# Kernel tuning notes

Measured on AMD Instinct MI355X. Metric: run time of the kernel, lower is better.

## Reference

```python
import jax, jax.numpy as jnp
import numpy as np

KEEP_RATIO = 0.5
B, H, W = 8, 1024, 1024


def setup_inputs() -> dict:
    key = jax.random.key(0)
    k1, k2, k3 = jax.random.split(key, 3)
    logits = jax.random.normal(k1, (B, 1, H, W), dtype=jnp.float32)
    targets = jax.random.randint(k2, (B, 1, H, W), 0, 2, dtype=jnp.int32)
    tissue_mask = jax.random.randint(k3, (B, 1, H, W), 0, 2, dtype=jnp.int32)
    return {"logits": logits, "targets": targets, "tissue_mask": tissue_mask}


def reference(logits, targets, tissue_mask):
    b = logits.shape[0]
    x = logits.reshape(b, -1)                       # (B, N)
    t = targets.reshape(b, -1).astype(x.dtype)      # {0,1}
    m = tissue_mask.reshape(b, -1).astype(x.dtype)  # {0,1}
    n = x.shape[1]

    # stable binary_cross_entropy_with_logits, reduction='none'
    bce = jnp.maximum(x, 0.0) - x * t + jnp.log1p(jnp.exp(-jnp.abs(x)))
    loss = bce * m                                  # masked per-pixel loss

    pos = t * m                                     # positives inside tissue
    neg = (1.0 - t) * m                             # negatives inside tissue
    n_pos = jnp.sum(pos, axis=1)                    # (B,)
    n_neg = jnp.sum(neg, axis=1)

    k_all = max(1, int(n * KEEP_RATIO))             # static python int
    # kept count per row: all positives + top-(k_all - n_pos) negatives (clamped)
    k_keep = n_pos + jnp.minimum(jnp.maximum(k_all - n_pos, 0.0), n_neg)  # (B,)

    BIG = jnp.asarray(1e30, x.dtype)
    # sort key: positives always first, then negatives by loss, then non-tissue
    sort_key = jnp.where(pos > 0, BIG, jnp.where(neg > 0, loss, -BIG))
    order = jnp.argsort(-sort_key, axis=1)          # descending
    sorted_loss = jnp.take_along_axis(loss, order, axis=1)

    ranks = jnp.arange(n, dtype=x.dtype)
    keep = (ranks[None, :] < k_keep[:, None]).astype(x.dtype)
    per_sample = jnp.sum(sorted_loss * keep, axis=1) / jnp.maximum(k_keep, 1.0)
    # fallback when no tissue pixels at all: torch keeps index 0 (loss there is 0)
    per_sample = jnp.where(k_keep > 0, per_sample, loss[:, 0])
    return jnp.mean(per_sample)
```

## Files before the change

kernel.cpp:

```cpp
#include <hip/hip_runtime.h>
#include <cstdint>
#include <cstddef>

#define N_PIX   1048576
#define B_ROWS  8
#define K_ALL   524288
#define WG_PER_ROW 256
#define ITERS   4
#define NBINS   2048
#define FPSCALE 262144.0f


__global__ __launch_bounds__(256, 6) void k_pass1(
    const float4* __restrict__ lg, const int4* __restrict__ tg, const int4* __restrict__ mk,
    unsigned long long* __restrict__ hist,
    unsigned* __restrict__ partNpos, double* __restrict__ partSpos, float* __restrict__ out)
{
    __shared__ unsigned long long hq[NBINS];
    __shared__ unsigned swp[4];
    __shared__ double   sws[4];
    const int tid = threadIdx.x;
    for (int b = tid; b < NBINS; b += 256) hq[b] = 0ull;
    if (blockIdx.x == 0 && tid == 0) *out = 0.f;

    const int r = blockIdx.x >> 8;
    const size_t base = (size_t)blockIdx.x * (ITERS * 256) + tid;

    float4 x[ITERS]; int4 t[ITERS]; int4 m[ITERS];
    #pragma unroll
    for (int i = 0; i < ITERS; ++i) {
        x[i] = lg[base + (size_t)i * 256];
        t[i] = tg[base + (size_t)i * 256];
        m[i] = mk[base + (size_t)i * 256];
    }
    __syncthreads();

    unsigned npos = 0; float spos = 0.f;

    auto proc = [&](float xx, int tt, int mm) {
        float ax = fabsf(xx);
        float e = __expf(-ax);
        float l = __logf(1.f + e);
        float bce = fmaxf(xx, 0.f) - xx * (float)tt + l;
        if (mm) {
            if (tt) { npos++; spos += bce; }
            else {
                unsigned bin = __float_as_uint(bce) >> 21;
                if (bin >= NBINS) bin = NBINS - 1;
                unsigned fx = (unsigned)__float2uint_rn(bce * FPSCALE);
                atomicAdd(&hq[bin], (1ull << 48) | (unsigned long long)fx);
            }
        }
    };

    #pragma unroll
    for (int i = 0; i < ITERS; ++i) {
        proc(x[i].x, t[i].x, m[i].x);
        proc(x[i].y, t[i].y, m[i].y);
        proc(x[i].z, t[i].z, m[i].z);
        proc(x[i].w, t[i].w, m[i].w);
    }

    for (int o = 32; o; o >>= 1) {
        npos += __shfl_down(npos, o);
        spos += __shfl_down(spos, o);
    }
    if ((tid & 63) == 0) { swp[tid >> 6] = npos; sws[tid >> 6] = (double)spos; }
    __syncthreads();
    if (tid == 0) {
        partNpos[blockIdx.x] = swp[0] + swp[1] + swp[2] + swp[3];
        partSpos[blockIdx.x] = sws[0] + sws[1] + sws[2] + sws[3];
    }

    unsigned long long* gh = hist + (size_t)r * NBINS;
    for (int b = tid; b < NBINS; b += 256) {
        unsigned long long v = hq[b];
        if (v) atomicAdd(&gh[b], v);
    }
}

__global__ __launch_bounds__(256) void k_final(
    const unsigned long long* __restrict__ hist,
    const unsigned* __restrict__ partNpos, const double* __restrict__ partSpos,
    float* __restrict__ out)
{
    __shared__ unsigned sc[2][256];
    __shared__ double   sd[2][256];
    __shared__ unsigned swp[4];
    __shared__ double   sws[4];
    __shared__ int rT; __shared__ unsigned rcntgt; __shared__ double rsumgt;

    const int r = blockIdx.x, tid = threadIdx.x;
    const unsigned long long* gh = hist + (size_t)r * NBINS;
    const double inv = 1.0 / (double)FPSCALE;

    {
        unsigned np = partNpos[r * 256 + tid];
        double   sp = partSpos[r * 256 + tid];
        for (int o = 32; o; o >>= 1) { np += __shfl_down(np, o); sp += __shfl_down(sp, o); }
        if ((tid & 63) == 0) { swp[tid >> 6] = np; sws[tid >> 6] = sp; }
    }
    __syncthreads();
    const unsigned npos = swp[0] + swp[1] + swp[2] + swp[3];
    const double sumPos = sws[0] + sws[1] + sws[2] + sws[3];
    __syncthreads();

    const int per = NBINS / 256;
    const int b0 = NBINS - 1 - tid * per;
    unsigned lc[8]; double lsum[8];
    unsigned pc = 0; double ps = 0.0;
    #pragma unroll
    for (int i = 0; i < per; ++i) {
        unsigned long long v = gh[b0 - i];
        lc[i] = (unsigned)(v >> 48);
        lsum[i] = (double)(v & 0xFFFFFFFFFFFFull) * inv;
        pc += lc[i]; ps += lsum[i];
    }

    int pp = 0;
    sc[0][tid] = pc; sd[0][tid] = ps;
    __syncthreads();
    for (int ofs = 1; ofs < 256; ofs <<= 1) {
        unsigned c = sc[pp][tid]; double s = sd[pp][tid];
        if (tid >= ofs) { c += sc[pp][tid - ofs]; s += sd[pp][tid - ofs]; }
        sc[pp ^ 1][tid] = c; sd[pp ^ 1][tid] = s;
        pp ^= 1;
        __syncthreads();
    }
    const unsigned nneg   = sc[pp][255];
    const double   sumNeg = sd[pp][255];

    long kl = (long)K_ALL - (long)npos;
    if (kl < 0) kl = 0;
    if (kl > (long)nneg) kl = (long)nneg;
    const unsigned Kneg = (unsigned)kl;

    double sum_sel = 0.0;
    if (Kneg >= nneg) {
        sum_sel = sumNeg;
    } else if (Kneg > 0) {
        unsigned inc = sc[pp][tid];
        unsigned exc = inc - pc;
        double   exs = sd[pp][tid] - ps;
        if (exc < Kneg && Kneg <= inc) {
            unsigned cum = exc; double csum = exs;
            #pragma unroll
            for (int i = 0; i < per; ++i) {
                if (cum + lc[i] >= Kneg) { rT = b0 - i; rcntgt = cum; rsumgt = csum; break; }
                cum += lc[i]; csum += lsum[i];
            }
        }
        __syncthreads();
        if (tid == 0) {
            const int T1 = rT;
            unsigned long long v = gh[T1];
            const unsigned cntT1 = (unsigned)(v >> 48);
            const double   sumT1 = (double)(v & 0xFFFFFFFFFFFFull) * inv;
            const unsigned Kp = Kneg - rcntgt;
            const float lo = __uint_as_float((unsigned)T1 << 21);
            const float hi = __uint_as_float((unsigned)(T1 + 1) << 21);
            const double w = (double)hi - (double)lo;
            const double avg = sumT1 / (double)cntT1;
            const double topmean = avg + 0.5 * w * (1.0 - (double)Kp / (double)cntT1);
            sum_sel = rsumgt + (double)Kp * topmean;
        }
    }

    if (tid == 0) {
        unsigned long long kk = (unsigned long long)npos + (unsigned long long)Kneg;
        double per_s = 0.0;
        if (kk > 0) per_s = (sumPos + sum_sel) / (double)kk;
        atomicAdd(out, (float)(per_s / (double)B_ROWS));
    }
}

extern "C" void kernel_launch(void* const* d_in, const int* in_sizes, int n_in,
                              void* d_out, int out_size, void* d_ws, size_t ws_size,
                              hipStream_t stream)
{
    const float* logits = (const float*)d_in[0];
    const int*   targets = (const int*)d_in[1];
    const int*   tissue = (const int*)d_in[2];

    const int NBLK = B_ROWS * WG_PER_ROW;
    char* ws = (char*)d_ws;
    size_t off = 0;
    unsigned long long* hist = (unsigned long long*)(ws + off);
    off += (size_t)B_ROWS * NBINS * 8;
    size_t zero_size = off;
    unsigned* partNpos = (unsigned*)(ws + off); off += (size_t)NBLK * 4;
    double*   partSpos = (double*)(ws + off);   off += (size_t)NBLK * 8;

    hipMemsetAsync(ws, 0, zero_size, stream);

    k_pass1<<<NBLK, 256, 0, stream>>>(
        (const float4*)logits, (const int4*)targets, (const int4*)tissue,
        hist, partNpos, partSpos, (float*)d_out);
    k_final<<<B_ROWS, 256, 0, stream>>>(hist, partNpos, partSpos, (float*)d_out);
}
```

Baseline: 122.9 us.

## Fuse histogram and final selection into one kernel via last-block-per-row

Merges the two kernels into one. The last workgroup of each row, found through an atomic counter, performs the histogram prefix scan and threshold selection, and the last row to finish writes the final mean. Per-block partials are replaced by per-row atomics, and the histogram is halved to 1024 bins with a repacked count/sum layout. This removes one kernel launch and the small serial final kernel, but makes the tail-bin approximation coarser and adds contended atomics and fences.

New measurement: 402.8 us. +227.6%, slower.

```diff
diff --git a/kernel.cpp b/kernel.cpp
--- a/kernel.cpp
+++ b/kernel.cpp
@@ -7,21 +7,30 @@
 #define K_ALL   524288
 #define WG_PER_ROW 256
 #define ITERS   4
-#define NBINS   2048
+#define NBINS   1024
+#define BSHIFT  22
+#define CSHIFT  40
+#define SUMMASK ((1ull << CSHIFT) - 1ull)
 #define FPSCALE 262144.0f
 
 
-__global__ __launch_bounds__(256, 6) void k_pass1(
+__global__ __launch_bounds__(256, 6) void k_fused(
     const float4* __restrict__ lg, const int4* __restrict__ tg, const int4* __restrict__ mk,
     unsigned long long* __restrict__ hist,
-    unsigned* __restrict__ partNpos, double* __restrict__ partSpos, float* __restrict__ out)
+    unsigned* __restrict__ rowNpos, double* __restrict__ rowSpos,
+    unsigned* __restrict__ rowCnt, unsigned* __restrict__ doneCnt,
+    double* __restrict__ rowPer, float* __restrict__ out)
 {
     __shared__ unsigned long long hq[NBINS];
     __shared__ unsigned swp[4];
     __shared__ double   sws[4];
+    __shared__ unsigned sc[2][256];
+    __shared__ double   sd[2][256];
+    __shared__ int rT; __shared__ unsigned rcntgt; __shared__ double rsumgt;
+    __shared__ int isLast;
+
     const int tid = threadIdx.x;
     for (int b = tid; b < NBINS; b += 256) hq[b] = 0ull;
-    if (blockIdx.x == 0 && tid == 0) *out = 0.f;
 
     const int r = blockIdx.x >> 8;
     const size_t base = (size_t)blockIdx.x * (ITERS * 256) + tid;
@@ -45,10 +54,10 @@
         if (mm) {
             if (tt) { npos++; spos += bce; }
             else {
-                unsigned bin = __float_as_uint(bce) >> 21;
+                unsigned bin = __float_as_uint(bce) >> BSHIFT;
                 if (bin >= NBINS) bin = NBINS - 1;
                 unsigned fx = (unsigned)__float2uint_rn(bce * FPSCALE);
-                atomicAdd(&hq[bin], (1ull << 48) | (unsigned long long)fx);
+                atomicAdd(&hq[bin], (1ull << CSHIFT) | (unsigned long long)fx);
             }
         }
     };
@@ -68,8 +77,10 @@
     if ((tid & 63) == 0) { swp[tid >> 6] = npos; sws[tid >> 6] = (double)spos; }
     __syncthreads();
     if (tid == 0) {
-        partNpos[blockIdx.x] = swp[0] + swp[1] + swp[2] + swp[3];
-        partSpos[blockIdx.x] = sws[0] + sws[1] + sws[2] + sws[3];
+        unsigned bn = swp[0] + swp[1] + swp[2] + swp[3];
+        double   bs = sws[0] + sws[1] + sws[2] + sws[3];
+        if (bn) atomicAdd(&rowNpos[r], bn);
+        if (bs != 0.0) atomicAdd(&rowSpos[r], bs);
     }
 
     unsigned long long* gh = hist + (size_t)r * NBINS;
@@ -77,43 +88,32 @@
         unsigned long long v = hq[b];
         if (v) atomicAdd(&gh[b], v);
     }
-}
-
-__global__ __launch_bounds__(256) void k_final(
-    const unsigned long long* __restrict__ hist,
-    const unsigned* __restrict__ partNpos, const double* __restrict__ partSpos,
-    float* __restrict__ out)
-{
-    __shared__ unsigned sc[2][256];
-    __shared__ double   sd[2][256];
-    __shared__ unsigned swp[4];
-    __shared__ double   sws[4];
-    __shared__ int rT; __shared__ unsigned rcntgt; __shared__ double rsumgt;
-
-    const int r = blockIdx.x, tid = threadIdx.x;
-    const unsigned long long* gh = hist + (size_t)r * NBINS;
+
+    __threadfence();
+    if (tid == 0) isLast = (atomicAdd(&rowCnt[r], 1u) == WG_PER_ROW - 1);
+    __syncthreads();
+    if (!isLast) return;
+    __threadfence();
+
     const double inv = 1.0 / (double)FPSCALE;
 
-    {
-        unsigned np = partNpos[r * 256 + tid];
-        double   sp = partSpos[r * 256 + tid];
-        for (int o = 32; o; o >>= 1) { np += __shfl_down(np, o); sp += __shfl_down(sp, o); }
-        if ((tid & 63) == 0) { swp[tid >> 6] = np; sws[tid >> 6] = sp; }
-    }
-    __syncthreads();
-    const unsigned npos = swp[0] + swp[1] + swp[2] + swp[3];
-    const double sumPos = sws[0] + sws[1] + sws[2] + sws[3];
-    __syncthreads();
+    if (tid == 0) {
+        swp[0] = atomicAdd(&rowNpos[r], 0u);
+        sws[0] = atomicAdd(&rowSpos[r], 0.0);
+    }
+    __syncthreads();
+    const unsigned nposR = swp[0];
+    const double  sumPos = sws[0];
 
     const int per = NBINS / 256;
     const int b0 = NBINS - 1 - tid * per;
-    unsigned lc[8]; double lsum[8];
+    unsigned lc[4]; double lsum[4];
     unsigned pc = 0; double ps = 0.0;
     #pragma unroll
     for (int i = 0; i < per; ++i) {
-        unsigned long long v = gh[b0 - i];
-        lc[i] = (unsigned)(v >> 48);
-        lsum[i] = (double)(v & 0xFFFFFFFFFFFFull) * inv;
+        unsigned long long v = atomicOr(&gh[b0 - i], 0ull);
+        lc[i] = (unsigned)(v >> CSHIFT);
+        lsum[i] = (double)(v & SUMMASK) * inv;
         pc += lc[i]; ps += lsum[i];
     }
 
@@ -130,7 +130,7 @@
     const unsigned nneg   = sc[pp][255];
     const double   sumNeg = sd[pp][255];
 
-    long kl = (long)K_ALL - (long)npos;
+    long kl = (long)K_ALL - (long)nposR;
     if (kl < 0) kl = 0;
     if (kl > (long)nneg) kl = (long)nneg;
     const unsigned Kneg = (unsigned)kl;
@@ -153,12 +153,12 @@
         __syncthreads();
         if (tid == 0) {
             const int T1 = rT;
-            unsigned long long v = gh[T1];
-            const unsigned cntT1 = (unsigned)(v >> 48);
-            const double   sumT1 = (double)(v & 0xFFFFFFFFFFFFull) * inv;
+            unsigned long long v = atomicOr(&gh[T1], 0ull);
+            const unsigned cntT1 = (unsigned)(v >> CSHIFT);
+            const double   sumT1 = (double)(v & SUMMASK) * inv;
             const unsigned Kp = Kneg - rcntgt;
-            const float lo = __uint_as_float((unsigned)T1 << 21);
-            const float hi = __uint_as_float((unsigned)(T1 + 1) << 21);
+            const float lo = __uint_as_float((unsigned)T1 << BSHIFT);
+            const float hi = __uint_as_float((unsigned)(T1 + 1) << BSHIFT);
             const double w = (double)hi - (double)lo;
             const double avg = sumT1 / (double)cntT1;
             const double topmean = avg + 0.5 * w * (1.0 - (double)Kp / (double)cntT1);
@@ -167,10 +167,18 @@
     }
 
     if (tid == 0) {
-        unsigned long long kk = (unsigned long long)npos + (unsigned long long)Kneg;
+        unsigned long long kk = (unsigned long long)nposR + (unsigned long long)Kneg;
         double per_s = 0.0;
         if (kk > 0) per_s = (sumPos + sum_sel) / (double)kk;
-        atomicAdd(out, (float)(per_s / (double)B_ROWS));
+        rowPer[r] = per_s;
+        __threadfence();
+        if (atomicAdd(doneCnt, 1u) == B_ROWS - 1) {
+            __threadfence();
+            double s = 0.0;
+            #pragma unroll
+            for (int i = 0; i < B_ROWS; ++i) s += atomicAdd(&rowPer[i], 0.0);
+            *out = (float)(s / (double)B_ROWS);
+        }
     }
 }
 
@@ -182,19 +190,20 @@
     const int*   targets = (const int*)d_in[1];
     const int*   tissue = (const int*)d_in[2];
 
-    const int NBLK = B_ROWS * WG_PER_ROW;
     char* ws = (char*)d_ws;
     size_t off = 0;
     unsigned long long* hist = (unsigned long long*)(ws + off);
     off += (size_t)B_ROWS * NBINS * 8;
-    size_t zero_size = off;
-    unsigned* partNpos = (unsigned*)(ws + off); off += (size_t)NBLK * 4;
-    double*   partSpos = (double*)(ws + off);   off += (size_t)NBLK * 8;
-
-    hipMemsetAsync(ws, 0, zero_size, stream);
-
-    k_pass1<<<NBLK, 256, 0, stream>>>(
+    double*   rowSpos = (double*)(ws + off);   off += B_ROWS * 8;
+    double*   rowPer  = (double*)(ws + off);   off += B_ROWS * 8;
+    unsigned* rowNpos = (unsigned*)(ws + off); off += B_ROWS * 4;
+    unsigned* rowCnt  = (unsigned*)(ws + off); off += B_ROWS * 4;
+    unsigned* doneCnt = (unsigned*)(ws + off); off += 4;
+
+    hipMemsetAsync(ws, 0, off, stream);
+
+    const int NBLK = B_ROWS * WG_PER_ROW;
+    k_fused<<<NBLK, 256, 0, stream>>>(
         (const float4*)logits, (const int4*)targets, (const int4*)tissue,
-        hist, partNpos, partSpos, (float*)d_out);
-    k_final<<<B_ROWS, 256, 0, stream>>>(hist, partNpos, partSpos, (float*)d_out);
+        hist, rowNpos, rowSpos, rowCnt, doneCnt, rowPer, (float*)d_out);
 }
```
